# Performance work log

Hardware: AMD Instinct MI355X
Metric: run time of the kernel (lower is better)

The kernel has to match this reference:

```python
import jax, jax.numpy as jnp
import numpy as np

IN_FEATURES = 4096
OUT_FEATURES = 8192
GROUP_SIZE = 16
NUM_GROUPS = IN_FEATURES * OUT_FEATURES // GROUP_SIZE  # 2_097_152


def block_dequantize_2bit(packed, normalization):
    # packed: [G, group_size//4] int32 holding uint8 values; norm: [G, 1] fp16
    shifts = jnp.arange(4, dtype=packed.dtype) * 2  # bit offsets 0,2,4,6
    # unpacked column 4k+i comes from packed column k, bits 2i..2i+1
    u = ((packed[:, :, None] >> shifts) & 3).astype(jnp.float32)  # [G, gs/4, 4]
    u = u.reshape(packed.shape[0], -1)  # [G, group_size]
    norm = normalization.astype(jnp.float32)
    return (u / 3.0) * (2.0 * norm) - norm  # [G, group_size]


def setup_inputs() -> dict:
    key = jax.random.key(0)
    k_x, k_q, k_n, k_b = jax.random.split(key, 4)
    x = jax.random.normal(k_x, (256, IN_FEATURES), dtype=jnp.float32)
    # packed 2-bit weights: random bytes (store as int32 for clean bit ops in jax)
    weight_q2 = jax.random.randint(k_q, (NUM_GROUPS, GROUP_SIZE // 4), 0, 256, dtype=jnp.int32)
    # per-group normalization (abs-max), positive, fp16 as in the module buffer
    weight_norm = (jax.random.uniform(k_n, (NUM_GROUPS, 1), dtype=jnp.float32) * 0.05 + 1e-4).astype(jnp.float16)
    bias = jax.random.normal(k_b, (OUT_FEATURES,), dtype=jnp.float32) * 0.01
    return {"x": x, "weight_q2": weight_q2, "weight_norm": weight_norm, "bias": bias}


def reference(x, weight_q2, weight_norm, bias):
    weight = block_dequantize_2bit(weight_q2, weight_norm).reshape(OUT_FEATURES, IN_FEATURES)
    return jnp.dot(x.astype(jnp.float32), weight.T) + bias
```

## Files before the change

kernel.cpp:

```cpp
#include <hip/hip_runtime.h>
#include <hip/hip_bf16.h>
#include <hip/hip_fp16.h>

#define IN_F   4096
#define OUT_F  8192
#define M_ROWS 256

typedef __attribute__((ext_vector_type(8))) short  short8;
typedef __attribute__((ext_vector_type(4))) float  float4v;

__device__ inline unsigned int pack_bf16(float lo, float hi) {
    return __builtin_amdgcn_perm(__float_as_uint(hi), __float_as_uint(lo), 0x07060302u);
}

__device__ inline int sw_idx(int row, int kchunk) {
    return row * 64 + ((kchunk ^ (row & 7)) << 3);
}

__global__ void cvt_x_kernel(const float* __restrict__ x, unsigned short* __restrict__ xb) {
    int i = blockIdx.x * blockDim.x + threadIdx.x;
    if (i < (M_ROWS * IN_F) / 4) {
        float4 v = ((const float4*)x)[i];
        uint2 o;
        o.x = pack_bf16(v.x, v.y);
        o.y = pack_bf16(v.z, v.w);
        ((uint2*)xb)[i] = o;
    }
}

__device__ inline void load_a16_f32(const float* __restrict__ p, uint4& o0, uint4& o1) {
    float4 v0 = ((const float4*)p)[0], v1 = ((const float4*)p)[1];
    float4 v2 = ((const float4*)p)[2], v3 = ((const float4*)p)[3];
    o0.x = pack_bf16(v0.x, v0.y); o0.y = pack_bf16(v0.z, v0.w);
    o0.z = pack_bf16(v1.x, v1.y); o0.w = pack_bf16(v1.z, v1.w);
    o1.x = pack_bf16(v2.x, v2.y); o1.y = pack_bf16(v2.z, v2.w);
    o1.z = pack_bf16(v3.x, v3.y); o1.w = pack_bf16(v3.z, v3.w);
}

template <bool XB>
__global__ __launch_bounds__(256, 2) void gemm2bit_kernel(
    const float*           __restrict__ xf,
    const unsigned short*  __restrict__ xb,
    const int*             __restrict__ wq,
    const void*            __restrict__ wnorm,
    const float*           __restrict__ bias,
    float*                 __restrict__ out)
{
    __shared__ unsigned short lds[2][2][64 * 64];

    const int t    = threadIdx.x;
    const int n0   = blockIdx.x * 64;
    const int m0   = blockIdx.y * 64;
    const int wave = t >> 6;
    const int lane = t & 63;
    const int l15  = lane & 15;
    const int quad = lane >> 4;
    const int wm   = (wave >> 1) * 32;
    const int wn   = (wave & 1) * 32;

    const float cand0 = *(const float*)wnorm;
    const bool  nf32  = (cand0 > 1e-5f && cand0 < 0.1f);

    const int srow = t >> 2;
    const int skc  = t & 3;
    const int c0   = skc * 2;
    const int wO0  = sw_idx(srow, c0);
    const int wO1  = sw_idx(srow, c0 + 1);

    int fa0[2], fa1[2], fb0[2], fb1[2];
#pragma unroll
    for (int kk = 0; kk < 2; ++kk) {
        fa0[kk] = sw_idx(wm +      l15, kk * 4 + quad);
        fa1[kk] = sw_idx(wm + 16 + l15, kk * 4 + quad);
        fb0[kk] = sw_idx(wn +      l15, kk * 4 + quad);
        fb1[kk] = sw_idx(wn + 16 + l15, kk * 4 + quad);
    }

    const int arow = m0 + srow;
    const int brow = n0 + srow;
    const float*          nrmF = (const float*)wnorm;
    const __half*         nrmH = (const __half*)wnorm;

    float4v acc[2][2] = {};

    uint4 aN0, aN1; int4 qN; float nN;
    {
        if (XB) {
            const unsigned short* p = xb + arow * IN_F + skc * 16;
            aN0 = *(const uint4*)p;
            aN1 = *(const uint4*)(p + 8);
        } else {
            load_a16_f32(xf + arow * IN_F + skc * 16, aN0, aN1);
        }
        qN = *(const int4*)(wq + brow * (IN_F / 4) + skc * 4);
        const int gi = brow * (IN_F / 16) + skc;
        nN = nf32 ? nrmF[gi] : __half2float(nrmH[gi]);
    }

    for (int ito = 0; ito < 32; ++ito) {
#pragma unroll
        for (int half = 0; half < 2; ++half) {
            const int it = ito * 2 + half;

            uint4 aC0 = aN0, aC1 = aN1;
            int4  qC  = qN;
            float nC  = nN;

            if (it < 63) {
                const int kn = (it + 1) << 6;
                if (XB) {
                    const unsigned short* p = xb + arow * IN_F + kn + skc * 16;
                    aN0 = *(const uint4*)p;
                    aN1 = *(const uint4*)(p + 8);
                } else {
                    load_a16_f32(xf + arow * IN_F + kn + skc * 16, aN0, aN1);
                }
                qN = *(const int4*)(wq + brow * (IN_F / 4) + (kn >> 2) + skc * 4);
                const int gi = brow * (IN_F / 16) + (kn >> 4) + skc;
                nN = nf32 ? nrmF[gi] : __half2float(nrmH[gi]);
            }

            const float s = nC * (2.0f / 3.0f);
            float f[16];
            const int qa[4] = {qC.x, qC.y, qC.z, qC.w};
#pragma unroll
            for (int bq = 0; bq < 4; ++bq) {
#pragma unroll
                for (int i = 0; i < 4; ++i)
                    f[bq * 4 + i] = fmaf((float)((qa[bq] >> (2 * i)) & 3), s, -nC);
            }
            uint4 bv0, bv1;
            bv0.x = pack_bf16(f[0],  f[1]);   bv0.y = pack_bf16(f[2],  f[3]);
            bv0.z = pack_bf16(f[4],  f[5]);   bv0.w = pack_bf16(f[6],  f[7]);
            bv1.x = pack_bf16(f[8],  f[9]);   bv1.y = pack_bf16(f[10], f[11]);
            bv1.z = pack_bf16(f[12], f[13]);  bv1.w = pack_bf16(f[14], f[15]);

            unsigned short* LA = lds[half][0];
            unsigned short* LB = lds[half][1];
            *(uint4*)&LA[wO0] = aC0;
            *(uint4*)&LA[wO1] = aC1;
            *(uint4*)&LB[wO0] = bv0;
            *(uint4*)&LB[wO1] = bv1;

            __syncthreads();

#pragma unroll
            for (int kk = 0; kk < 2; ++kk) {
                short8 a0 = *(const short8*)&LA[fa0[kk]];
                short8 a1 = *(const short8*)&LA[fa1[kk]];
                short8 b0 = *(const short8*)&LB[fb0[kk]];
                short8 b1 = *(const short8*)&LB[fb1[kk]];
                acc[0][0] = __builtin_amdgcn_mfma_f32_16x16x32_bf16(a0, b0, acc[0][0], 0, 0, 0);
                acc[0][1] = __builtin_amdgcn_mfma_f32_16x16x32_bf16(a0, b1, acc[0][1], 0, 0, 0);
                acc[1][0] = __builtin_amdgcn_mfma_f32_16x16x32_bf16(a1, b0, acc[1][0], 0, 0, 0);
                acc[1][1] = __builtin_amdgcn_mfma_f32_16x16x32_bf16(a1, b1, acc[1][1], 0, 0, 0);
            }
        }
    }

#pragma unroll
    for (int j = 0; j < 2; ++j) {
        const int col = n0 + wn + j * 16 + l15;
        const float bv = bias[col];
#pragma unroll
        for (int i = 0; i < 2; ++i) {
            const int row0 = m0 + wm + i * 16 + quad * 4;
#pragma unroll
            for (int r = 0; r < 4; ++r) {
                out[(row0 + r) * OUT_F + col] = acc[i][j][r] + bv;
            }
        }
    }
}

extern "C" void kernel_launch(void* const* d_in, const int* in_sizes, int n_in,
                              void* d_out, int out_size, void* d_ws, size_t ws_size,
                              hipStream_t stream) {
    const float*          x    = (const float*)d_in[0];
    const int*            wq   = (const int*)d_in[1];
    const void*           wn   = (const void*)d_in[2];
    const float*          bias = (const float*)d_in[3];
    float*                out  = (float*)d_out;

    const bool use_ws = ws_size >= (size_t)(M_ROWS * IN_F * sizeof(unsigned short));

    dim3 grid(OUT_F / 64, M_ROWS / 64);

    if (use_ws) {
        unsigned short* xb = (unsigned short*)d_ws;
        cvt_x_kernel<<<dim3((M_ROWS * IN_F / 4 + 255) / 256), 256, 0, stream>>>(x, xb);
        gemm2bit_kernel<true><<<grid, 256, 0, stream>>>(nullptr, xb, wq, wn, bias, out);
    } else {
        gemm2bit_kernel<false><<<grid, 256, 0, stream>>>(x, nullptr, wq, wn, bias, out);
    }
}
```

Before: 130.7 us.

## Split K across four blocks with atomic accumulation into bias-initialized output

Adds a split-K dimension of four to the grid, so each block covers a quarter of the reduction and adds its partial result into the output with atomicAdd. A new init kernel first writes the bias into the output. Launch bounds are raised to 4 blocks per CU to fit the larger grid. The gain sought is more blocks in flight to cover the dequant and load latency of the 2-bit weights. The cost is 4x the output traffic as atomics, an extra 8 MB init pass, and results that are no longer bit-deterministic.

```diff
diff --git a/kernel.cpp b/kernel.cpp
--- a/kernel.cpp
+++ b/kernel.cpp
@@ -5,6 +5,10 @@
 #define IN_F   4096
 #define OUT_F  8192
 #define M_ROWS 256
+
+#define SPLITK 4
+#define K_SPL  (IN_F / SPLITK)
+#define NIT    (K_SPL / 64)
 
 typedef __attribute__((ext_vector_type(8))) short  short8;
 typedef __attribute__((ext_vector_type(4))) float  float4v;
@@ -28,6 +32,14 @@
     }
 }
 
+__global__ void init_out_kernel(const float* __restrict__ bias, float* __restrict__ out) {
+    int i = blockIdx.x * blockDim.x + threadIdx.x;
+    if (i < (M_ROWS * OUT_F) / 4) {
+        float4 b = ((const float4*)bias)[i & (OUT_F / 4 - 1)];
+        ((float4*)out)[i] = b;
+    }
+}
+
 __device__ inline void load_a16_f32(const float* __restrict__ p, uint4& o0, uint4& o1) {
     float4 v0 = ((const float4*)p)[0], v1 = ((const float4*)p)[1];
     float4 v2 = ((const float4*)p)[2], v3 = ((const float4*)p)[3];
@@ -38,12 +50,11 @@
 }
 
 template <bool XB>
-__global__ __launch_bounds__(256, 2) void gemm2bit_kernel(
+__global__ __launch_bounds__(256, 4) void gemm2bit_kernel(
     const float*           __restrict__ xf,
     const unsigned short*  __restrict__ xb,
     const int*             __restrict__ wq,
     const void*            __restrict__ wnorm,
-    const float*           __restrict__ bias,
     float*                 __restrict__ out)
 {
     __shared__ unsigned short lds[2][2][64 * 64];
@@ -51,6 +62,7 @@
     const int t    = threadIdx.x;
     const int n0   = blockIdx.x * 64;
     const int m0   = blockIdx.y * 64;
+    const int kb   = blockIdx.z * K_SPL;
     const int wave = t >> 6;
     const int lane = t & 63;
     const int l15  = lane & 15;
@@ -86,18 +98,18 @@
     uint4 aN0, aN1; int4 qN; float nN;
     {
         if (XB) {
-            const unsigned short* p = xb + arow * IN_F + skc * 16;
+            const unsigned short* p = xb + arow * IN_F + kb + skc * 16;
             aN0 = *(const uint4*)p;
             aN1 = *(const uint4*)(p + 8);
         } else {
-            load_a16_f32(xf + arow * IN_F + skc * 16, aN0, aN1);
+            load_a16_f32(xf + arow * IN_F + kb + skc * 16, aN0, aN1);
         }
-        qN = *(const int4*)(wq + brow * (IN_F / 4) + skc * 4);
-        const int gi = brow * (IN_F / 16) + skc;
+        qN = *(const int4*)(wq + brow * (IN_F / 4) + (kb >> 2) + skc * 4);
+        const int gi = brow * (IN_F / 16) + (kb >> 4) + skc;
         nN = nf32 ? nrmF[gi] : __half2float(nrmH[gi]);
     }
 
-    for (int ito = 0; ito < 32; ++ito) {
+    for (int ito = 0; ito < NIT / 2; ++ito) {
 #pragma unroll
         for (int half = 0; half < 2; ++half) {
             const int it = ito * 2 + half;
@@ -106,8 +118,8 @@
             int4  qC  = qN;
             float nC  = nN;
 
-            if (it < 63) {
-                const int kn = (it + 1) << 6;
+            if (it < NIT - 1) {
+                const int kn = kb + ((it + 1) << 6);
                 if (XB) {
                     const unsigned short* p = xb + arow * IN_F + kn + skc * 16;
                     aN0 = *(const uint4*)p;
@@ -161,13 +173,12 @@
 #pragma unroll
     for (int j = 0; j < 2; ++j) {
         const int col = n0 + wn + j * 16 + l15;
-        const float bv = bias[col];
 #pragma unroll
         for (int i = 0; i < 2; ++i) {
             const int row0 = m0 + wm + i * 16 + quad * 4;
 #pragma unroll
             for (int r = 0; r < 4; ++r) {
-                out[(row0 + r) * OUT_F + col] = acc[i][j][r] + bv;
+                atomicAdd(&out[(row0 + r) * OUT_F + col], acc[i][j][r]);
             }
         }
     }
@@ -184,13 +195,15 @@
 
     const bool use_ws = ws_size >= (size_t)(M_ROWS * IN_F * sizeof(unsigned short));
 
-    dim3 grid(OUT_F / 64, M_ROWS / 64);
+    dim3 grid(OUT_F / 64, M_ROWS / 64, SPLITK);
+
+    init_out_kernel<<<dim3((M_ROWS * OUT_F / 4) / 256), 256, 0, stream>>>(bias, out);
 
     if (use_ws) {
         unsigned short* xb = (unsigned short*)d_ws;
         cvt_x_kernel<<<dim3((M_ROWS * IN_F / 4 + 255) / 256), 256, 0, stream>>>(x, xb);
-        gemm2bit_kernel<true><<<grid, 256, 0, stream>>>(nullptr, xb, wq, wn, bias, out);
+        gemm2bit_kernel<true><<<grid, 256, 0, stream>>>(nullptr, xb, wq, wn, out);
     } else {
-        gemm2bit_kernel<false><<<grid, 256, 0, stream>>>(x, nullptr, wq, wn, bias, out);
-    }
-}
+        gemm2bit_kernel<false><<<grid, 256, 0, stream>>>(x, nullptr, wq, wn, out);
+    }
+}
```

Measured after the change: 133.2 us. About the same (+1.9%).
